# Kernel optimization log

Measured on AMD Instinct MI355X. Metric: run time of the kernel, lower is better.

The kernel has to match this reference:

```python
import jax, jax.numpy as jnp
import numpy as np

B, K, M, MN = 256, 32, 64, 256
E, H, Q = 128, 128, 128
NE, NR, NNODES = 100000, 500, 256  # entities, relations, max_nodes


def setup_inputs() -> dict:
    key = jax.random.key(0)
    ks = jax.random.split(key, 24)
    f = lambda k, s: jax.random.normal(k, s, jnp.float32) * 0.05
    inp = {}
    inp['start_entities'] = jax.random.randint(ks[0], (B,), 0, NE)
    inp['aims'] = jax.random.randint(ks[1], (B, K), 0, NE)
    inp['node_pos'] = jnp.broadcast_to(jnp.arange(1, K + 1, dtype=jnp.int32), (B, K))
    inp['neighbor_nodes'] = jax.random.randint(ks[2], (B, K, M), 0, NNODES)
    inp['neighbor_relations'] = jax.random.randint(ks[3], (B, K, M), 0, NR)
    inp['neighbors_num'] = jax.random.randint(ks[4], (B, K), 0, M + 1)
    inp['currents'] = jax.random.randint(ks[5], (B,), 0, NNODES)
    inp['candidate_nodes'] = jax.random.randint(ks[6], (B, MN), 0, NNODES)
    inp['candidate_entities'] = jax.random.randint(ks[7], (B, MN), 0, NE)
    inp['candidate_relations'] = jax.random.randint(ks[8], (B, MN), 0, NR)
    inp['candidate_masks'] = jax.random.randint(ks[9], (B, MN), 0, 2).astype(bool)
    inp['entity_emb'] = f(ks[10], (NE, E))
    inp['relation_emb'] = f(ks[11], (NR, E))
    inp['hidden_W'] = f(ks[12], (H, E)); inp['hidden_b'] = f(ks[13], (H,))
    inp['pass_W'] = f(ks[14], (H, H + E)); inp['pass_b'] = f(ks[15], (H,))
    inp['nexthop_W'] = f(ks[16], (H, H + Q)); inp['nexthop_b'] = f(ks[17], (H,))
    inp['candidate_W'] = f(ks[18], (H, H + 2 * E)); inp['candidate_b'] = f(ks[19], (H,))
    inp['gate_W'] = f(ks[20], (1, H + Q)); inp['gate_b'] = f(ks[21], (1,))
    inp['query'] = f(ks[22], (B, Q))
    return inp


def _linear(x, W, b):
    return x @ W.T + b


def _lrelu(x):
    return jax.nn.leaky_relu(x, 0.01)  # torch LeakyReLU default


def _gather_nodes(node_emb, idx):
    # node_emb: (B, N+2, H), idx: (B, ...) -> (B, ..., H)
    b = node_emb.shape[0]
    g = jnp.take_along_axis(node_emb, idx.reshape(b, -1)[:, :, None], axis=1)
    return g.reshape(*idx.shape, node_emb.shape[-1])


def reference(start_entities, aims, node_pos, neighbor_nodes, neighbor_relations,
              neighbors_num, currents, candidate_nodes, candidate_entities,
              candidate_relations, candidate_masks, entity_emb, relation_emb,
              hidden_W, hidden_b, pass_W, pass_b, nexthop_W, nexthop_b,
              candidate_W, candidate_b, gate_W, gate_b, query):
    # ---- Agent.init ----
    node_emb = jnp.zeros((B, NNODES + 2, H), jnp.float32)
    init = _lrelu(_linear(entity_emb[start_entities], hidden_W, hidden_b))
    node_emb = node_emb.at[:, 0].set(init)
    # ---- Agent.aggregate: gather -> Linear -> masked mean -> scatter ----
    aim_e = entity_emb[aims]                                   # (B,K,E)
    nb_node = _gather_nodes(node_emb, neighbor_nodes)          # (B,K,M,H)
    nb_rel = relation_emb[neighbor_relations]                  # (B,K,M,E)
    nb = _linear(jnp.concatenate([nb_node, nb_rel], -1), pass_W, pass_b)  # pass_activation = identity
    keep = jnp.arange(M) < neighbors_num[:, :, None]           # (B,K,M)
    nb = jnp.where(keep[..., None], nb, 0.0)
    denom = (neighbors_num + (neighbors_num == 0)).astype(jnp.float32)
    agg = nb.sum(axis=2) / denom[..., None]                    # (B,K,H)
    upd = _lrelu(_linear(aim_e, hidden_W, hidden_b) + agg)
    node_emb = node_emb.at[jnp.arange(B)[:, None], node_pos].set(upd)
    # ---- Agent.next_hop ----
    cur = _gather_nodes(node_emb, currents)                    # (B,H)
    cur_cat = jnp.concatenate([cur, query], axis=1)            # (B,H+Q)
    state = _lrelu(_linear(cur_cat, nexthop_W, nexthop_b))     # (B,H)
    cnode = _gather_nodes(node_emb, candidate_nodes)           # (B,MN,H)
    cand = _lrelu(_linear(jnp.concatenate(
        [cnode, entity_emb[candidate_entities], relation_emb[candidate_relations]], -1),
        candidate_W, candidate_b))                             # (B,MN,H)
    thresh = _linear(cur_cat, gate_W, gate_b)                  # (B,1)
    scores = jnp.einsum('bh,bmh->bm', state, cand) / jnp.sqrt(jnp.float32(E))
    scores = jnp.where(candidate_masks, scores, jnp.float32(-100000.0))
    final_scores = jnp.concatenate([scores, thresh], axis=1)   # (B,MN+1)
    return final_scores
```

## Files before the change

### kernel.cpp

```cpp
#include <hip/hip_runtime.h>

#define B 256
#define K 32
#define M 64
#define MN 256
#define E 128
#define H 128
#define Q 128
#define NSLOT 258
#define CTILE 32
#define XPAD 392

typedef __attribute__((ext_vector_type(8))) short short8;
typedef __attribute__((ext_vector_type(4))) short short4b;
typedef __attribute__((ext_vector_type(4))) float f32x4;

__device__ __forceinline__ float lrelu(float x){ return x >= 0.f ? x : 0.01f*x; }

__device__ __forceinline__ unsigned short f2bf(float f){
    unsigned int u = __float_as_uint(f);
    unsigned int r = u + 0x7FFFu + ((u >> 16) & 1u);
    return (unsigned short)(r >> 16);
}

__device__ __forceinline__ short4b pack4(float4 v){
    short4b r;
    r.x = (short)f2bf(v.x); r.y = (short)f2bf(v.y);
    r.z = (short)f2bf(v.z); r.w = (short)f2bf(v.w);
    return r;
}

__device__ __forceinline__ short8 f8_from(const float* __restrict__ p){
    float4 u = *(const float4*)p;
    float4 v = *(const float4*)(p + 4);
    short8 s;
    s[0]=(short)f2bf(u.x); s[1]=(short)f2bf(u.y); s[2]=(short)f2bf(u.z); s[3]=(short)f2bf(u.w);
    s[4]=(short)f2bf(v.x); s[5]=(short)f2bf(v.y); s[6]=(short)f2bf(v.z); s[7]=(short)f2bf(v.w);
    return s;
}

__global__ void k_front(const int* __restrict__ aims, const int* __restrict__ nbr_nodes,
                        const int* __restrict__ nbr_rels, const int* __restrict__ nbr_num,
                        const int* __restrict__ start_ent, const int* __restrict__ node_pos,
                        const float* __restrict__ ent_emb, const float* __restrict__ rel_emb,
                        const float* __restrict__ hW, const float* __restrict__ hb,
                        const float* __restrict__ passW, const float* __restrict__ candW,
                        float* __restrict__ ab, int* __restrict__ map,
                        float* __restrict__ init_out, float* __restrict__ wninit_out,
                        unsigned short* __restrict__ Wf, unsigned short* __restrict__ Wcatf,
                        unsigned short* __restrict__ Pf,
                        unsigned short* __restrict__ XhG, unsigned short* __restrict__ XaG){
    int blk = blockIdx.x, t = threadIdx.x;
    __shared__ float e[128];
    __shared__ float si[128];
    __shared__ unsigned int hist[4][512];
    __shared__ float sden[4];

    if (blk >= 848) {
        int hb4 = blk - 848;
        for (int i = t; i < 2048; i += 256) ((unsigned int*)hist)[i] = 0u;
        __syncthreads();
        int w = t >> 6, lane = t & 63;
        int bk = hb4*4 + w;
        int num = nbr_num[bk];
        int nr  = nbr_rels[(long)bk*M + lane];
        int nn  = nbr_nodes[(long)bk*M + lane];
        unsigned long long mask = __ballot((lane < num) && (nn == 0));
        int c0 = (int)__popcll(mask);
        float denom = (float)(num > 0 ? num : 1);
        if (lane < num) atomicAdd(&hist[w][nr], 1u);
        float2 av = *(const float2*)&ent_emb[(long)aims[bk]*E + lane*2];
        ushort2 ap; ap.x = f2bf(av.x); ap.y = f2bf(av.y);
        *(ushort2*)&XaG[(long)bk*128 + lane*2] = ap;
        if (lane == 0) {
            ab[bk*2+0] = (float)c0 / denom;
            ab[bk*2+1] = (float)num / denom;
            sden[w] = 1.f / denom;
        }
        __syncthreads();
        for (int i = t; i < 2048; i += 256) {
            int w2 = i >> 9, r = i & 511;
            float v = (float)hist[w2][r] * sden[w2];
            XhG[((long)(hb4*4 + w2))*512 + r] = f2bf(v);
        }
        return;
    }

    int pb = blk;
    if (pb < 256) {
        int b = pb;
        if (t < 128) e[t] = ent_emb[(long)start_ent[b]*E + t];
        __syncthreads();
        if (t < 128) {
            float acc = hb[t];
            #pragma unroll 8
            for (int j=0;j<E;j++) acc += hW[t*E+j]*e[j];
            float v = lrelu(acc);
            si[t] = v;
            init_out[b*H+t] = v;
        }
        __syncthreads();
        if (t < 128) {
            float acc2 = 0.f;
            #pragma unroll 8
            for (int j=0;j<H;j++) acc2 += passW[t*(H+E)+j]*si[j];
            wninit_out[b*H+t] = acc2;
        }
    } else if (pb < 512) {
        int b = pb - 256;
        for (int i=t;i<NSLOT;i+=256) map[b*NSLOT+i] = -2;
        __syncthreads();
        if (t==0) map[b*NSLOT+0] = -1;
        __syncthreads();
        if (t<K) map[b*NSLOT + node_pos[b*K+t]] = t;
    } else if (pb < 704) {
        int i = (pb-512)*256 + t;
        int j = i & 7;
        int l = (i >> 3) & 63;
        int ct = (i >> 9) & 1;
        int r = i >> 10;
        int ks = r % 12, w = r / 12;
        int row = w*32 + ct*16 + (l & 15);
        int col = ks*32 + (l >> 4)*8 + j;
        Wf[i] = f2bf(candW[row*384 + col]);
    } else if (pb < 832) {
        int i = (pb-704)*256 + t;
        int j = i & 7;
        int l = (i >> 3) & 63;
        int ct = (i >> 9) & 1;
        int r = i >> 10;
        int ks = r & 7, w = r >> 3;
        int row = w*32 + ct*16 + (l & 15);
        int col = ks*32 + (l >> 4)*8 + j;
        float v = (col < 128) ? passW[row*256 + 128 + col] : hW[row*128 + (col-128)];
        Wcatf[i] = f2bf(v);
    } else {
        int g = pb - 832;
        int w = t >> 6, lane = t & 63;
        int l16 = lane & 15, lhi = lane >> 4;
        int hbase = w*32;
        const short8 z8 = (short8){0,0,0,0,0,0,0,0};
        f32x4 acc[2][2];
        #pragma unroll
        for (int rt=0;rt<2;rt++)
            #pragma unroll
            for (int ct=0;ct<2;ct++)
                acc[rt][ct] = (f32x4){0.f,0.f,0.f,0.f};
        #pragma unroll
        for (int ks2 = 0; ks2 < 4; ks2++) {
            int kof = ks2*32 + lhi*8;
            int r0 = g*32 + l16, r1 = g*32 + 16 + l16;
            short8 a0 = (r0 < 500) ? f8_from(&rel_emb[(long)r0*E + kof]) : z8;
            short8 a1 = (r1 < 500) ? f8_from(&rel_emb[(long)r1*E + kof]) : z8;
            short8 b0 = f8_from(&passW[(long)(hbase + l16)*(H+E) + H + kof]);
            short8 b1 = f8_from(&passW[(long)(hbase + 16 + l16)*(H+E) + H + kof]);
            acc[0][0] = __builtin_amdgcn_mfma_f32_16x16x32_bf16(a0, b0, acc[0][0], 0, 0, 0);
            acc[0][1] = __builtin_amdgcn_mfma_f32_16x16x32_bf16(a0, b1, acc[0][1], 0, 0, 0);
            acc[1][0] = __builtin_amdgcn_mfma_f32_16x16x32_bf16(a1, b0, acc[1][0], 0, 0, 0);
            acc[1][1] = __builtin_amdgcn_mfma_f32_16x16x32_bf16(a1, b1, acc[1][1], 0, 0, 0);
        }
        #pragma unroll
        for (int rt=0; rt<2; rt++) {
            #pragma unroll
            for (int ct=0; ct<2; ct++) {
                #pragma unroll
                for (int i=0;i<4;i++) {
                    int rp = rt*16 + 4*lhi + i;
                    long idx = ((long)((w*16 + g)*2 + ct))*512 + (l16 + (rp>>3)*16)*8 + (rp & 7);
                    Pf[idx] = f2bf(acc[rt][ct][i]);
                }
            }
        }
    }
}

__global__ void k_updg(const unsigned short* __restrict__ XhG,
                       const unsigned short* __restrict__ XaG,
                       const float* __restrict__ ab,
                       const unsigned short* __restrict__ Wcatf,
                       const unsigned short* __restrict__ Pf,
                       const float* __restrict__ hb_, const float* __restrict__ passb,
                       const float* __restrict__ wninit,
                       const int* __restrict__ currents, const int* __restrict__ map,
                       const float* __restrict__ init, const float* __restrict__ query,
                       const float* __restrict__ nW, const float* __restrict__ nb_,
                       const float* __restrict__ gW, const float* __restrict__ gb,
                       float* __restrict__ upd, float* __restrict__ state,
                       float* __restrict__ out){
    int b = blockIdx.x;
    int t = threadIdx.x;
    __shared__ __align__(16) unsigned short Xh[32][520];
    __shared__ __align__(16) unsigned short Xa[32][136];
    __shared__ float wni[128];
    __shared__ float sab[64];
    __shared__ float cc[H+Q];
    __shared__ float wsum[2];
    #pragma unroll
    for (int it = 0; it < 8; it++) {
        int idx = it*256 + t;
        int r = idx >> 6;
        int cg = (idx & 63) * 8;
        *(short8*)&Xh[r][cg] = *(const short8*)&XhG[((long)b*32 + r)*512 + cg];
    }
    #pragma unroll
    for (int it = 0; it < 2; it++) {
        int idx = it*256 + t;
        int r = idx >> 4;
        int cg = (idx & 15) * 8;
        *(short8*)&Xa[r][cg] = *(const short8*)&XaG[((long)b*32 + r)*128 + cg];
    }
    if (t < 128) wni[t] = wninit[b*128 + t];
    else if (t < 192) sab[t-128] = ab[b*64 + (t-128)];

    int w    = t >> 6;
    int lane = t & 63;
    int l16  = lane & 15;
    int lhi  = lane >> 4;
    int hbase = w*32;
    int mvc = map[b*NSLOT + currents[b]];
    __syncthreads();

    f32x4 acc[2][2];
    #pragma unroll
    for (int rt=0;rt<2;rt++)
        #pragma unroll
        for (int ct=0;ct<2;ct++)
            acc[rt][ct] = (f32x4){0.f,0.f,0.f,0.f};

    #pragma unroll 4
    for (int ks = 0; ks < 16; ks++) {
        int kof = ks*32 + lhi*8;
        short8 a0 = *(const short8*)&Xh[l16][kof];
        short8 a1 = *(const short8*)&Xh[16 + l16][kof];
        short8 b0 = *(const short8*)&Pf[(((long)(w*16+ks)*2 + 0)*64 + lane)*8];
        short8 b1 = *(const short8*)&Pf[(((long)(w*16+ks)*2 + 1)*64 + lane)*8];
        acc[0][0] = __builtin_amdgcn_mfma_f32_16x16x32_bf16(a0, b0, acc[0][0], 0, 0, 0);
        acc[0][1] = __builtin_amdgcn_mfma_f32_16x16x32_bf16(a0, b1, acc[0][1], 0, 0, 0);
        acc[1][0] = __builtin_amdgcn_mfma_f32_16x16x32_bf16(a1, b0, acc[1][0], 0, 0, 0);
        acc[1][1] = __builtin_amdgcn_mfma_f32_16x16x32_bf16(a1, b1, acc[1][1], 0, 0, 0);
    }
    #pragma unroll
    for (int ks2 = 0; ks2 < 4; ks2++) {
        int kof = ks2*32 + lhi*8;
        short8 a0 = *(const short8*)&Xa[l16][kof];
        short8 a1 = *(const short8*)&Xa[16 + l16][kof];
        short8 b0 = *(const short8*)&Wcatf[((((w*8 + 4 + ks2)*2 + 0)*64) + lane)*8];
        short8 b1 = *(const short8*)&Wcatf[((((w*8 + 4 + ks2)*2 + 1)*64) + lane)*8];
        acc[0][0] = __builtin_amdgcn_mfma_f32_16x16x32_bf16(a0, b0, acc[0][0], 0, 0, 0);
        acc[0][1] = __builtin_amdgcn_mfma_f32_16x16x32_bf16(a0, b1, acc[0][1], 0, 0, 0);
        acc[1][0] = __builtin_amdgcn_mfma_f32_16x16x32_bf16(a1, b0, acc[1][0], 0, 0, 0);
        acc[1][1] = __builtin_amdgcn_mfma_f32_16x16x32_bf16(a1, b1, acc[1][1], 0, 0, 0);
    }

    int h0 = hbase + l16, h1 = hbase + 16 + l16;
    float hb0 = hb_[h0], hb1 = hb_[h1];
    float pb0 = passb[h0], pb1 = passb[h1];
    float w0 = wni[h0],  w1 = wni[h1];

    if (t < 128) {
        cc[t] = (mvc == -1) ? init[b*H + t] : 0.f;
        cc[H+t] = query[b*Q + t];
    }

    float uv[2][2][4];
    #pragma unroll
    for (int rt=0; rt<2; rt++) {
        #pragma unroll
        for (int i=0;i<4;i++) {
            int r = rt*16 + 4*lhi + i;
            float al = sab[r*2], be = sab[r*2+1];
            float v0 = lrelu(hb0 + al*w0 + be*pb0 + acc[rt][0][i]);
            float v1 = lrelu(hb1 + al*w1 + be*pb1 + acc[rt][1][i]);
            uv[rt][0][i] = v0; uv[rt][1][i] = v1;
            upd[((long)b*32 + r)*128 + h0] = v0;
            upd[((long)b*32 + r)*128 + h1] = v1;
        }
    }
    __syncthreads();
    if (mvc >= 0) {
        #pragma unroll
        for (int rt=0; rt<2; rt++) {
            #pragma unroll
            for (int i=0;i<4;i++) {
                int r = rt*16 + 4*lhi + i;
                if (r == mvc) { cc[h0] = uv[rt][0][i]; cc[h1] = uv[rt][1][i]; }
            }
        }
    }
    __syncthreads();

    if (t < 128) {
        float sacc = nb_[t];
        #pragma unroll 8
        for (int j=0;j<H+Q;j++) sacc += nW[t*(H+Q)+j]*cc[j];
        state[b*H+t] = lrelu(sacc);
        float tv = gW[t]*cc[t] + gW[H+t]*cc[H+t];
        for (int off=32; off>0; off>>=1) tv += __shfl_down(tv, off);
        if ((t&63)==0) wsum[t>>6] = tv;
    }
    __syncthreads();
    if (t==0) out[b*(MN+1) + MN] = wsum[0] + wsum[1] + gb[0];
}

__global__ __launch_bounds__(256, 2)
void k_cand(const int* __restrict__ cnodes, const int* __restrict__ cents,
            const int* __restrict__ crels, const int* __restrict__ cmask,
            const int* __restrict__ map,
            const float* __restrict__ init, const float* __restrict__ upd,
            const float* __restrict__ ent_emb, const float* __restrict__ rel_emb,
            const unsigned short* __restrict__ Wf, const float* __restrict__ cb,
            const float* __restrict__ state,
            float* __restrict__ out){
    int blk = blockIdx.x;
    int b  = blk >> 1;
    int cbase = (blk & 1) * 128;
    int t  = threadIdx.x;

    __shared__ __align__(16) unsigned short Xb[CTILE][XPAD];
    __shared__ float sscore[4][CTILE];
    __shared__ int sce[128], scr[128], smv[128];

    if (t < 128) {
        int row = b*MN + cbase + t;
        sce[t] = cents[row];
        scr[t] = crels[row];
        smv[t] = map[b*NSLOT + cnodes[row]];
    }

    int w    = t >> 6;
    int lane = t & 63;
    int l16  = lane & 15;
    int lhi  = lane >> 4;
    int c8   = t >> 5;
    int q    = t & 31;

    short8 bw[12][2];
    #pragma unroll
    for (int ks = 0; ks < 12; ks++) {
        #pragma unroll
        for (int ct = 0; ct < 2; ct++)
            bw[ks][ct] = *(const short8*)&Wf[((((w*12+ks)*2+ct)*64) + lane)*8];
    }
    float s0  = state[b*H + w*32 + l16];
    float s1  = state[b*H + w*32 + 16 + l16];
    float cb0 = cb[w*32 + l16];
    float cb1 = cb[w*32 + 16 + l16];
    __syncthreads();

    #pragma unroll
    for (int tile = 0; tile < 4; ++tile) {
        #pragma unroll
        for (int i = 0; i < 4; i++) {
            int ci = tile*32 + i*8 + c8;
            int cl = i*8 + c8;
            int mv = smv[ci];
            float4 nv = {0.f,0.f,0.f,0.f};
            if (mv == -1)      nv = *(const float4*)&init[b*H + q*4];
            else if (mv >= 0)  nv = *(const float4*)&upd[((long)b*K+mv)*H + q*4];
            float4 ev = *(const float4*)&ent_emb[(long)sce[ci]*E + q*4];
            float4 rv = *(const float4*)&rel_emb[(long)scr[ci]*E + q*4];
            *(short4b*)&Xb[cl][q*4]       = pack4(nv);
            *(short4b*)&Xb[cl][128 + q*4] = pack4(ev);
            *(short4b*)&Xb[cl][256 + q*4] = pack4(rv);
        }
        __syncthreads();

        f32x4 acc[2][2];
        #pragma unroll
        for (int rt=0;rt<2;rt++)
            #pragma unroll
            for (int ct=0;ct<2;ct++)
                acc[rt][ct] = (f32x4){0.f,0.f,0.f,0.f};

        #pragma unroll
        for (int ks = 0; ks < 12; ks++) {
            int kof = ks*32 + lhi*8;
            short8 a0 = *(const short8*)&Xb[l16][kof];
            short8 a1 = *(const short8*)&Xb[16 + l16][kof];
            acc[0][0] = __builtin_amdgcn_mfma_f32_16x16x32_bf16(a0, bw[ks][0], acc[0][0], 0, 0, 0);
            acc[0][1] = __builtin_amdgcn_mfma_f32_16x16x32_bf16(a0, bw[ks][1], acc[0][1], 0, 0, 0);
            acc[1][0] = __builtin_amdgcn_mfma_f32_16x16x32_bf16(a1, bw[ks][0], acc[1][0], 0, 0, 0);
            acc[1][1] = __builtin_amdgcn_mfma_f32_16x16x32_bf16(a1, bw[ks][1], acc[1][1], 0, 0, 0);
        }

        #pragma unroll
        for (int rt=0; rt<2; rt++) {
            float ps[4];
            #pragma unroll
            for (int i=0;i<4;i++)
                ps[i] = lrelu(acc[rt][0][i] + cb0)*s0 + lrelu(acc[rt][1][i] + cb1)*s1;
            #pragma unroll
            for (int msk=1; msk<16; msk<<=1) {
                #pragma unroll
                for (int i=0;i<4;i++) ps[i] += __shfl_xor(ps[i], msk);
            }
            if (l16 == 0) {
                #pragma unroll
                for (int i=0;i<4;i++)
                    sscore[w][rt*16 + 4*lhi + i] = ps[i];
            }
        }
        __syncthreads();

        if (t < CTILE) {
            int row = b*MN + cbase + tile*32 + t;
            float s = (sscore[0][t] + sscore[1][t] + sscore[2][t] + sscore[3][t])
                      * 0.08838834764831845f;
            out[b*(MN+1) + cbase + tile*32 + t] = cmask[row] ? s : -100000.0f;
        }
    }
}

extern "C" void kernel_launch(void* const* d_in, const int* in_sizes, int n_in,
                              void* d_out, int out_size, void* d_ws, size_t ws_size,
                              hipStream_t stream){
    (void)in_sizes; (void)n_in; (void)out_size; (void)ws_size;
    const int* start_entities      = (const int*)d_in[0];
    const int* aims                = (const int*)d_in[1];
    const int* node_pos            = (const int*)d_in[2];
    const int* neighbor_nodes      = (const int*)d_in[3];
    const int* neighbor_relations  = (const int*)d_in[4];
    const int* neighbors_num       = (const int*)d_in[5];
    const int* currents            = (const int*)d_in[6];
    const int* candidate_nodes     = (const int*)d_in[7];
    const int* candidate_entities  = (const int*)d_in[8];
    const int* candidate_relations = (const int*)d_in[9];
    const int* candidate_masks     = (const int*)d_in[10];
    const float* entity_emb   = (const float*)d_in[11];
    const float* relation_emb = (const float*)d_in[12];
    const float* hidden_W     = (const float*)d_in[13];
    const float* hidden_b     = (const float*)d_in[14];
    const float* pass_W       = (const float*)d_in[15];
    const float* pass_b       = (const float*)d_in[16];
    const float* nexthop_W    = (const float*)d_in[17];
    const float* nexthop_b    = (const float*)d_in[18];
    const float* candidate_W  = (const float*)d_in[19];
    const float* candidate_b  = (const float*)d_in[20];
    const float* gate_W       = (const float*)d_in[21];
    const float* gate_b       = (const float*)d_in[22];
    const float* query        = (const float*)d_in[23];
    float* out = (float*)d_out;

    float* ws     = (float*)d_ws;
    float* init   = ws;
    float* wninit = init + B*H;
    float* upd    = wninit + B*H;
    float* state  = upd + (long)B*K*H;
    float* ab     = state + B*H;
    int*   map    = (int*)(ab + B*K*2);
    unsigned short* Wf    = (unsigned short*)(map + B*NSLOT);
    unsigned short* Wcatf = Wf + 49152;
    unsigned short* Pf    = Wcatf + 32768;
    unsigned short* XhG   = Pf + 65536;
    unsigned short* XaG   = XhG + (long)B*K*512;

    k_front<<<848 + (B*K)/4, 256, 0, stream>>>(aims, neighbor_nodes, neighbor_relations,
                                               neighbors_num, start_entities, node_pos,
                                               entity_emb, relation_emb,
                                               hidden_W, hidden_b, pass_W, candidate_W,
                                               ab, map, init, wninit, Wf, Wcatf,
                                               Pf, XhG, XaG);
    k_updg<<<B, 256, 0, stream>>>(XhG, XaG, ab, Wcatf, Pf, hidden_b, pass_b, wninit,
                                  currents, map, init, query,
                                  nexthop_W, nexthop_b, gate_W, gate_b,
                                  upd, state, out);
    k_cand<<<2*B, 256, 0, stream>>>(candidate_nodes, candidate_entities,
                                    candidate_relations, candidate_masks,
                                    map, init, upd, entity_emb, relation_emb,
                                    Wf, candidate_b, state, out);
}
```

Measured before the change: 54.07 us.

## Split k_cand into one block per 32-candidate tile with branchless batched gathers

k_cand now launches eight blocks per batch row, each handling a single 32-candidate tile, instead of two blocks each looping over four tiles. The node-embedding gather now picks its pointer without branching, using a zeroed row in the workspace (written by k_front) as the fallback. All twelve loads are issued before any packing, so more gathers are in flight at once. The weight fragments are now read from global memory inside the MFMA loop rather than held in registers across tiles. The aim is more parallelism and memory-level overlap for the latency-bound gathers, at the cost of each block reloading the weights and dropping the launch-bounds hint.

```diff
diff --git a/kernel.cpp b/kernel.cpp
--- a/kernel.cpp
+++ b/kernel.cpp
@@ -49,7 +49,8 @@
                         float* __restrict__ init_out, float* __restrict__ wninit_out,
                         unsigned short* __restrict__ Wf, unsigned short* __restrict__ Wcatf,
                         unsigned short* __restrict__ Pf,
-                        unsigned short* __restrict__ XhG, unsigned short* __restrict__ XaG){
+                        unsigned short* __restrict__ XhG, unsigned short* __restrict__ XaG,
+                        float* __restrict__ zrow){
     int blk = blockIdx.x, t = threadIdx.x;
     __shared__ float e[128];
     __shared__ float si[128];
@@ -113,6 +114,7 @@
         if (t==0) map[b*NSLOT+0] = -1;
         __syncthreads();
         if (t<K) map[b*NSLOT + node_pos[b*K+t]] = t;
+        if (pb == 256 && t < 128) zrow[t] = 0.f;
     } else if (pb < 704) {
         int i = (pb-512)*256 + t;
         int j = i & 7;
@@ -302,112 +304,117 @@
     if (t==0) out[b*(MN+1) + MN] = wsum[0] + wsum[1] + gb[0];
 }
 
-__global__ __launch_bounds__(256, 2)
-void k_cand(const int* __restrict__ cnodes, const int* __restrict__ cents,
-            const int* __restrict__ crels, const int* __restrict__ cmask,
-            const int* __restrict__ map,
-            const float* __restrict__ init, const float* __restrict__ upd,
-            const float* __restrict__ ent_emb, const float* __restrict__ rel_emb,
-            const unsigned short* __restrict__ Wf, const float* __restrict__ cb,
-            const float* __restrict__ state,
-            float* __restrict__ out){
+__global__ void k_cand(const int* __restrict__ cnodes, const int* __restrict__ cents,
+                       const int* __restrict__ crels, const int* __restrict__ cmask,
+                       const int* __restrict__ map,
+                       const float* __restrict__ init, const float* __restrict__ upd,
+                       const float* __restrict__ ent_emb, const float* __restrict__ rel_emb,
+                       const unsigned short* __restrict__ Wf, const float* __restrict__ cb,
+                       const float* __restrict__ state, const float* __restrict__ zrow,
+                       float* __restrict__ out){
     int blk = blockIdx.x;
-    int b  = blk >> 1;
-    int cbase = (blk & 1) * 128;
+    int b  = blk >> 3;
+    int c0 = (blk & 7) * CTILE;
     int t  = threadIdx.x;
 
     __shared__ __align__(16) unsigned short Xb[CTILE][XPAD];
     __shared__ float sscore[4][CTILE];
-    __shared__ int sce[128], scr[128], smv[128];
-
-    if (t < 128) {
-        int row = b*MN + cbase + t;
+    __shared__ int sce[CTILE], scr[CTILE], smv[CTILE];
+
+    if (t < CTILE) {
+        int row = b*MN + c0 + t;
         sce[t] = cents[row];
         scr[t] = crels[row];
         smv[t] = map[b*NSLOT + cnodes[row]];
+    }
+    __syncthreads();
+
+    {
+        int c8 = t >> 5;
+        int q  = t & 31;
+        const float* pn[4]; const float* pe[4]; const float* pr[4];
+        #pragma unroll
+        for (int i = 0; i < 4; i++) {
+            int c = i*8 + c8;
+            int mv = smv[c];
+            const float* bs = zrow;
+            bs = (mv == -1) ? (init + (long)b*H) : bs;
+            bs = (mv >= 0)  ? (upd + ((long)b*K + mv)*H) : bs;
+            pn[i] = bs + q*4;
+            pe[i] = ent_emb + (long)sce[c]*E + q*4;
+            pr[i] = rel_emb + (long)scr[c]*E + q*4;
+        }
+        float4 vn[4], ve[4], vr[4];
+        #pragma unroll
+        for (int i = 0; i < 4; i++) vn[i] = *(const float4*)pn[i];
+        #pragma unroll
+        for (int i = 0; i < 4; i++) ve[i] = *(const float4*)pe[i];
+        #pragma unroll
+        for (int i = 0; i < 4; i++) vr[i] = *(const float4*)pr[i];
+        #pragma unroll
+        for (int i = 0; i < 4; i++) {
+            int cl = i*8 + c8;
+            *(short4b*)&Xb[cl][q*4]       = pack4(vn[i]);
+            *(short4b*)&Xb[cl][128 + q*4] = pack4(ve[i]);
+            *(short4b*)&Xb[cl][256 + q*4] = pack4(vr[i]);
+        }
     }
 
     int w    = t >> 6;
     int lane = t & 63;
     int l16  = lane & 15;
     int lhi  = lane >> 4;
-    int c8   = t >> 5;
-    int q    = t & 31;
-
-    short8 bw[12][2];
-    #pragma unroll
-    for (int ks = 0; ks < 12; ks++) {
-        #pragma unroll
-        for (int ct = 0; ct < 2; ct++)
-            bw[ks][ct] = *(const short8*)&Wf[((((w*12+ks)*2+ct)*64) + lane)*8];
-    }
-    float s0  = state[b*H + w*32 + l16];
-    float s1  = state[b*H + w*32 + 16 + l16];
+
+    float s0 = state[b*H + w*32 + l16];
+    float s1 = state[b*H + w*32 + 16 + l16];
     float cb0 = cb[w*32 + l16];
     float cb1 = cb[w*32 + 16 + l16];
     __syncthreads();
 
-    #pragma unroll
-    for (int tile = 0; tile < 4; ++tile) {
-        #pragma unroll
-        for (int i = 0; i < 4; i++) {
-            int ci = tile*32 + i*8 + c8;
-            int cl = i*8 + c8;
-            int mv = smv[ci];
-            float4 nv = {0.f,0.f,0.f,0.f};
-            if (mv == -1)      nv = *(const float4*)&init[b*H + q*4];
-            else if (mv >= 0)  nv = *(const float4*)&upd[((long)b*K+mv)*H + q*4];
-            float4 ev = *(const float4*)&ent_emb[(long)sce[ci]*E + q*4];
-            float4 rv = *(const float4*)&rel_emb[(long)scr[ci]*E + q*4];
-            *(short4b*)&Xb[cl][q*4]       = pack4(nv);
-            *(short4b*)&Xb[cl][128 + q*4] = pack4(ev);
-            *(short4b*)&Xb[cl][256 + q*4] = pack4(rv);
-        }
-        __syncthreads();
-
-        f32x4 acc[2][2];
-        #pragma unroll
-        for (int rt=0;rt<2;rt++)
+    f32x4 acc[2][2];
+    #pragma unroll
+    for (int rt=0;rt<2;rt++)
+        #pragma unroll
+        for (int ct=0;ct<2;ct++)
+            acc[rt][ct] = (f32x4){0.f,0.f,0.f,0.f};
+
+    #pragma unroll
+    for (int ks = 0; ks < 12; ks++) {
+        int kof = ks*32 + lhi*8;
+        short8 b0 = *(const short8*)&Wf[((((w*12+ks)*2+0)*64) + lane)*8];
+        short8 b1 = *(const short8*)&Wf[((((w*12+ks)*2+1)*64) + lane)*8];
+        short8 a0 = *(const short8*)&Xb[l16][kof];
+        short8 a1 = *(const short8*)&Xb[16 + l16][kof];
+        acc[0][0] = __builtin_amdgcn_mfma_f32_16x16x32_bf16(a0, b0, acc[0][0], 0, 0, 0);
+        acc[0][1] = __builtin_amdgcn_mfma_f32_16x16x32_bf16(a0, b1, acc[0][1], 0, 0, 0);
+        acc[1][0] = __builtin_amdgcn_mfma_f32_16x16x32_bf16(a1, b0, acc[1][0], 0, 0, 0);
+        acc[1][1] = __builtin_amdgcn_mfma_f32_16x16x32_bf16(a1, b1, acc[1][1], 0, 0, 0);
+    }
+
+    #pragma unroll
+    for (int rt=0; rt<2; rt++) {
+        float ps[4];
+        #pragma unroll
+        for (int i=0;i<4;i++)
+            ps[i] = lrelu(acc[rt][0][i] + cb0)*s0 + lrelu(acc[rt][1][i] + cb1)*s1;
+        #pragma unroll
+        for (int msk=1; msk<16; msk<<=1) {
             #pragma unroll
-            for (int ct=0;ct<2;ct++)
-                acc[rt][ct] = (f32x4){0.f,0.f,0.f,0.f};
-
-        #pragma unroll
-        for (int ks = 0; ks < 12; ks++) {
-            int kof = ks*32 + lhi*8;
-            short8 a0 = *(const short8*)&Xb[l16][kof];
-            short8 a1 = *(const short8*)&Xb[16 + l16][kof];
-            acc[0][0] = __builtin_amdgcn_mfma_f32_16x16x32_bf16(a0, bw[ks][0], acc[0][0], 0, 0, 0);
-            acc[0][1] = __builtin_amdgcn_mfma_f32_16x16x32_bf16(a0, bw[ks][1], acc[0][1], 0, 0, 0);
-            acc[1][0] = __builtin_amdgcn_mfma_f32_16x16x32_bf16(a1, bw[ks][0], acc[1][0], 0, 0, 0);
-            acc[1][1] = __builtin_amdgcn_mfma_f32_16x16x32_bf16(a1, bw[ks][1], acc[1][1], 0, 0, 0);
-        }
-
-        #pragma unroll
-        for (int rt=0; rt<2; rt++) {
-            float ps[4];
+            for (int i=0;i<4;i++) ps[i] += __shfl_xor(ps[i], msk);
+        }
+        if (l16 == 0) {
             #pragma unroll
             for (int i=0;i<4;i++)
-                ps[i] = lrelu(acc[rt][0][i] + cb0)*s0 + lrelu(acc[rt][1][i] + cb1)*s1;
-            #pragma unroll
-            for (int msk=1; msk<16; msk<<=1) {
-                #pragma unroll
-                for (int i=0;i<4;i++) ps[i] += __shfl_xor(ps[i], msk);
-            }
-            if (l16 == 0) {
-                #pragma unroll
-                for (int i=0;i<4;i++)
-                    sscore[w][rt*16 + 4*lhi + i] = ps[i];
-            }
-        }
-        __syncthreads();
-
-        if (t < CTILE) {
-            int row = b*MN + cbase + tile*32 + t;
-            float s = (sscore[0][t] + sscore[1][t] + sscore[2][t] + sscore[3][t])
-                      * 0.08838834764831845f;
-            out[b*(MN+1) + cbase + tile*32 + t] = cmask[row] ? s : -100000.0f;
-        }
+                sscore[w][rt*16 + 4*lhi + i] = ps[i];
+        }
+    }
+    __syncthreads();
+
+    if (t < CTILE) {
+        int row = b*MN + c0 + t;
+        float s = (sscore[0][t] + sscore[1][t] + sscore[2][t] + sscore[3][t])
+                  * 0.08838834764831845f;
+        out[b*(MN+1) + c0 + t] = cmask[row] ? s : -100000.0f;
     }
 }
 
@@ -447,7 +454,8 @@
     float* upd    = wninit + B*H;
     float* state  = upd + (long)B*K*H;
     float* ab     = state + B*H;
-    int*   map    = (int*)(ab + B*K*2);
+    float* zrow   = ab + B*K*2;
+    int*   map    = (int*)(zrow + 128);
     unsigned short* Wf    = (unsigned short*)(map + B*NSLOT);
     unsigned short* Wcatf = Wf + 49152;
     unsigned short* Pf    = Wcatf + 32768;
@@ -459,13 +467,13 @@
                                                entity_emb, relation_emb,
                                                hidden_W, hidden_b, pass_W, candidate_W,
                                                ab, map, init, wninit, Wf, Wcatf,
-                                               Pf, XhG, XaG);
+                                               Pf, XhG, XaG, zrow);
     k_updg<<<B, 256, 0, stream>>>(XhG, XaG, ab, Wcatf, Pf, hidden_b, pass_b, wninit,
                                   currents, map, init, query,
                                   nexthop_W, nexthop_b, gate_W, gate_b,
                                   upd, state, out);
-    k_cand<<<2*B, 256, 0, stream>>>(candidate_nodes, candidate_entities,
-                                    candidate_relations, candidate_masks,
-                                    map, init, upd, entity_emb, relation_emb,
-                                    Wf, candidate_b, state, out);
-}
+    k_cand<<<B*(MN/CTILE), 256, 0, stream>>>(candidate_nodes, candidate_entities,
+                                             candidate_relations, candidate_masks,
+                                             map, init, upd, entity_emb, relation_emb,
+                                             Wf, candidate_b, state, zrow, out);
+}
```

Measured after the change: 50.23 us. -7.1%, faster.
